# Kernel optimization log

Hardware: AMD Instinct MI355X
Metric: run time of the kernel (lower is better)

Reference implementation:

```python
import jax, jax.numpy as jnp
import numpy as np

B, S, D, H, HD, P = 2, 2048, 1024, 16, 64, 512  # batch, seq, d_model, heads, head_dim, max_pos


def setup_inputs() -> dict:
    key = jax.random.key(0)
    ks = jax.random.split(key, 7)
    s = 1.0 / np.sqrt(D)
    return {
        "hidden_states": jax.random.normal(ks[0], (B, S, D), jnp.float32),
        "Wq": jax.random.normal(ks[1], (D, D), jnp.float32) * s,
        "Wk": jax.random.normal(ks[2], (D, D), jnp.float32) * s,
        "Wv": jax.random.normal(ks[3], (D, D), jnp.float32) * s,
        "Wo": jax.random.normal(ks[4], (D, D), jnp.float32) * s,
        "bo": jnp.full((D,), 0.1, jnp.float32),
        "pos_emb": jax.random.normal(ks[5], (2 * P + 1, H), jnp.float32) * 0.02,
    }


def reference(hidden_states, Wq, Wk, Wv, Wo, bo, pos_emb):
    x = hidden_states
    b, s, d = x.shape
    # QKV projections (no bias), split heads -> [b, s, H, HD]
    q = jnp.einsum("bsd,de->bse", x, Wq).reshape(b, s, H, HD)
    k = jnp.einsum("bsd,de->bse", x, Wk).reshape(b, s, H, HD)
    v = jnp.einsum("bsd,de->bse", x, Wv).reshape(b, s, H, HD)
    # scores [b, H, i, j]
    scores = jnp.einsum("bihd,bjhd->bhij", q, k) / np.sqrt(HD) + 1e-9
    # learned relative-position bias: rel[i,j] = clamp(j - i, -P, P) + P
    pos = jnp.arange(s)
    rel = jnp.clip(pos[None, :] - pos[:, None], -P, P) + P  # [s, s] int
    bias = pos_emb[rel]  # [s, s, H]
    scores = scores + jnp.transpose(bias, (2, 0, 1))[None]  # [1,H,s,s] broadcast
    # causal mask (strict upper triangle -> -inf)
    causal = jnp.triu(jnp.ones((s, s), bool), 1)
    scores = jnp.where(causal[None, None], -jnp.inf, scores)
    probs = jax.nn.softmax(scores, axis=-1)
    # attn dropout = 0 (eval). Weighted sum over values, merge heads.
    out = jnp.einsum("bhij,bjhd->bihd", probs, v).reshape(b, s, d)
    return jnp.einsum("bsd,de->bse", out, Wo) + bo
```

## Files before the change

kernel.cpp:

```cpp
#include <hip/hip_runtime.h>
#include <math.h>

#define SEQ    2048
#define DMODEL 1024
#define NHEAD  16
#define HDIM   64
#define MAXP   512
#define NBATCH 2
#define MTOT   (NBATCH * SEQ)
#define PAD    72
#define NT     (SEQ / 64)

typedef short s16x8 __attribute__((ext_vector_type(8)));
typedef float f32x4 __attribute__((ext_vector_type(4)));

__device__ __forceinline__ unsigned short f2bf(float f) {
    unsigned u = __float_as_uint(f);
    return (unsigned short)((u + 0x7FFFu + ((u >> 16) & 1u)) >> 16);
}
__device__ __forceinline__ float bf2f(unsigned short h) {
    return __uint_as_float(((unsigned)h) << 16);
}
__device__ __forceinline__ void tsplit(float v, unsigned short& hi, unsigned short& lo) {
    unsigned u = __float_as_uint(v);
    hi = (unsigned short)(u >> 16);
    float rem = v - __uint_as_float(u & 0xFFFF0000u);
    lo = (unsigned short)(__float_as_uint(rem) >> 16);
}

__global__ __launch_bounds__(256) void split_rows(
    const float* __restrict__ in, unsigned short* __restrict__ hi,
    unsigned short* __restrict__ lo, int n4)
{
    int i = blockIdx.x * 256 + threadIdx.x;
    if (i >= n4) return;
    float4 v = ((const float4*)in)[i];
    ushort4 h, l;
    h.x = f2bf(v.x); l.x = f2bf(v.x - bf2f(h.x));
    h.y = f2bf(v.y); l.y = f2bf(v.y - bf2f(h.y));
    h.z = f2bf(v.z); l.z = f2bf(v.z - bf2f(h.z));
    h.w = f2bf(v.w); l.w = f2bf(v.w - bf2f(h.w));
    ((ushort4*)hi)[i] = h;
    ((ushort4*)lo)[i] = l;
}

__global__ __launch_bounds__(256) void split_transpose(
    const float* __restrict__ W, unsigned short* __restrict__ th,
    unsigned short* __restrict__ tl)
{
    __shared__ float tile[32][33];
    const int bx = blockIdx.x * 32;
    const int by = blockIdx.y * 32;
    const int tx = threadIdx.x & 31, ty0 = threadIdx.x >> 5;
    #pragma unroll
    for (int i = 0; i < 4; ++i) {
        int ty = ty0 + i * 8;
        tile[ty][tx] = W[(size_t)(by + ty) * DMODEL + bx + tx];
    }
    __syncthreads();
    #pragma unroll
    for (int i = 0; i < 4; ++i) {
        int ty = ty0 + i * 8;
        float v = tile[tx][ty];
        unsigned short h = f2bf(v);
        unsigned short l = f2bf(v - bf2f(h));
        size_t o = (size_t)(bx + ty) * DMODEL + by + tx;
        th[o] = h;
        tl[o] = l;
    }
}

__global__ __launch_bounds__(256, 2) void gemm_mfma(
    const unsigned short* __restrict__ Ah_g, const unsigned short* __restrict__ Al_g,
    const unsigned short* __restrict__ Bh_g, const unsigned short* __restrict__ Bl_g,
    const float* __restrict__ bias, float* __restrict__ Yf,
    unsigned short* __restrict__ Yh, unsigned short* __restrict__ Yl, int mode)
{
    __shared__ __align__(16) unsigned short Ah[128 * 32], Al[128 * 32];
    __shared__ __align__(16) unsigned short Bh[128 * 32], Bl[128 * 32];

    const int tid = threadIdx.x;
    const int lane = tid & 63, wid = tid >> 6;
    const int wr = wid >> 1, wc = wid & 1;
    const int m0 = blockIdx.y * 128, n0 = blockIdx.x * 128;

    const int srow = tid >> 2;
    const int skb = (tid & 3) * 8;
    const size_t aoff0 = (size_t)(m0 + srow) * DMODEL + skb;
    const size_t aoff1 = (size_t)(m0 + srow + 64) * DMODEL + skb;
    const size_t boff0 = (size_t)(n0 + srow) * DMODEL + skb;
    const size_t boff1 = (size_t)(n0 + srow + 64) * DMODEL + skb;
    const int lw = srow * 32 + skb;

    uint4 rah0 = *(const uint4*)(Ah_g + aoff0), rah1 = *(const uint4*)(Ah_g + aoff1);
    uint4 ral0 = *(const uint4*)(Al_g + aoff0), ral1 = *(const uint4*)(Al_g + aoff1);
    uint4 rbh0 = *(const uint4*)(Bh_g + boff0), rbh1 = *(const uint4*)(Bh_g + boff1);
    uint4 rbl0 = *(const uint4*)(Bl_g + boff0), rbl1 = *(const uint4*)(Bl_g + boff1);

    f32x4 acc[4][4] = {};

    const int fr = lane & 15;
    const int fk = (lane >> 4) * 8;

    for (int t = 0; t < DMODEL / 32; ++t) {
        __syncthreads();
        *(uint4*)&Ah[lw] = rah0; *(uint4*)&Ah[lw + 64 * 32] = rah1;
        *(uint4*)&Al[lw] = ral0; *(uint4*)&Al[lw + 64 * 32] = ral1;
        *(uint4*)&Bh[lw] = rbh0; *(uint4*)&Bh[lw + 64 * 32] = rbh1;
        *(uint4*)&Bl[lw] = rbl0; *(uint4*)&Bl[lw + 64 * 32] = rbl1;
        __syncthreads();
        if (t + 1 < DMODEL / 32) {
            const size_t ko = (size_t)(t + 1) * 32;
            rah0 = *(const uint4*)(Ah_g + aoff0 + ko);
            rah1 = *(const uint4*)(Ah_g + aoff1 + ko);
            ral0 = *(const uint4*)(Al_g + aoff0 + ko);
            ral1 = *(const uint4*)(Al_g + aoff1 + ko);
            rbh0 = *(const uint4*)(Bh_g + boff0 + ko);
            rbh1 = *(const uint4*)(Bh_g + boff1 + ko);
            rbl0 = *(const uint4*)(Bl_g + boff0 + ko);
            rbl1 = *(const uint4*)(Bl_g + boff1 + ko);
        }

        s16x8 fah[4], fal[4], fbh[4], fbl[4];
        #pragma unroll
        for (int mf = 0; mf < 4; ++mf) {
            int r = (wr * 64 + mf * 16 + fr) * 32 + fk;
            fah[mf] = *(const s16x8*)&Ah[r];
            fal[mf] = *(const s16x8*)&Al[r];
        }
        #pragma unroll
        for (int nf = 0; nf < 4; ++nf) {
            int r = (wc * 64 + nf * 16 + fr) * 32 + fk;
            fbh[nf] = *(const s16x8*)&Bh[r];
            fbl[nf] = *(const s16x8*)&Bl[r];
        }
        __builtin_amdgcn_s_setprio(1);
        #pragma unroll
        for (int mf = 0; mf < 4; ++mf)
            #pragma unroll
            for (int nf = 0; nf < 4; ++nf) {
                acc[mf][nf] = __builtin_amdgcn_mfma_f32_16x16x32_bf16(fah[mf], fbh[nf], acc[mf][nf], 0, 0, 0);
                acc[mf][nf] = __builtin_amdgcn_mfma_f32_16x16x32_bf16(fah[mf], fbl[nf], acc[mf][nf], 0, 0, 0);
                acc[mf][nf] = __builtin_amdgcn_mfma_f32_16x16x32_bf16(fal[mf], fbh[nf], acc[mf][nf], 0, 0, 0);
            }
        __builtin_amdgcn_s_setprio(0);
    }

    #pragma unroll
    for (int mf = 0; mf < 4; ++mf) {
        #pragma unroll
        for (int nf = 0; nf < 4; ++nf) {
            const int col = n0 + wc * 64 + nf * 16 + fr;
            if (mode == 2) {
                const int hh = col >> 6, d = col & 63;
                const int row0 = m0 + wr * 64 + mf * 16 + (lane >> 4) * 4;
                const int bb = row0 >> 11, ss = row0 & (SEQ - 1);
                const size_t idx = (((size_t)bb * NHEAD + hh) * HDIM + d) * SEQ + ss;
                ushort4 hv, lv;
                {
                    float v0 = acc[mf][nf][0], v1 = acc[mf][nf][1];
                    float v2 = acc[mf][nf][2], v3 = acc[mf][nf][3];
                    hv.x = f2bf(v0); lv.x = f2bf(v0 - bf2f(hv.x));
                    hv.y = f2bf(v1); lv.y = f2bf(v1 - bf2f(hv.y));
                    hv.z = f2bf(v2); lv.z = f2bf(v2 - bf2f(hv.z));
                    hv.w = f2bf(v3); lv.w = f2bf(v3 - bf2f(hv.w));
                }
                *(ushort4*)(Yh + idx) = hv;
                *(ushort4*)(Yl + idx) = lv;
            } else {
                #pragma unroll
                for (int r = 0; r < 4; ++r) {
                    const int row = m0 + wr * 64 + mf * 16 + (lane >> 4) * 4 + r;
                    const float v = acc[mf][nf][r];
                    if (mode == 0) {
                        const int hh = col >> 6, d = col & 63;
                        const int bb = row >> 11, ss = row & (SEQ - 1);
                        size_t idx = ((((size_t)bb * NHEAD + hh) * SEQ + ss) << 6) + d;
                        unsigned short hb = f2bf(v);
                        Yh[idx] = hb;
                        Yl[idx] = f2bf(v - bf2f(hb));
                    } else {
                        Yf[(size_t)row * DMODEL + col] = v + bias[col];
                    }
                }
            }
        }
    }
}

__global__ __launch_bounds__(256, 2) void attn_mfma(
    const unsigned short* __restrict__ Qh_g, const unsigned short* __restrict__ Ql_g,
    const unsigned short* __restrict__ Kh_g, const unsigned short* __restrict__ Kl_g,
    const unsigned short* __restrict__ Vth_g, const unsigned short* __restrict__ Vtl_g,
    const float* __restrict__ pos_emb,
    unsigned short* __restrict__ Oh_g, unsigned short* __restrict__ Ol_g)
{
    __shared__ __align__(16) unsigned short kph[64 * PAD];
    __shared__ __align__(16) unsigned short kpl[64 * PAD];
    __shared__ __align__(16) unsigned short vth[64 * PAD];
    __shared__ __align__(16) unsigned short vtl[64 * PAD];
    __shared__ float pe[2 * MAXP + 1];

    const int tid = threadIdx.x;
    const int lane = tid & 63, w = tid >> 6;
    const int pi = blockIdx.x, bh = blockIdx.y;
    const int b = bh >> 4, h = bh & 15;

    const size_t hboff = ((size_t)b * NHEAD + h) * SEQ * HDIM;
    const unsigned short* Qh = Qh_g + hboff;
    const unsigned short* Ql = Ql_g + hboff;
    const unsigned short* Kh = Kh_g + hboff;
    const unsigned short* Kl = Kl_g + hboff;
    const unsigned short* Vth = Vth_g + hboff;
    const unsigned short* Vtl = Vtl_g + hboff;

    for (int e = tid; e <= 2 * MAXP; e += 256)
        pe[e] = pos_emb[(size_t)e * NHEAD + h];

    const int fr = lane & 15;
    const int g = lane >> 4;
    const int fko = g * 8;

    const int strow = tid >> 3;
    const int std0 = (tid & 7) * 8;

    uint4 rkh0, rkh1, rkl0, rkl1, rvh0, rvh1, rvl0, rvl1;
#define LDREGS(J0) do {                                                         \
    const unsigned short* kp_ = Kh + (size_t)((J0) + strow) * HDIM + std0;      \
    rkh0 = *(const uint4*)kp_;  rkh1 = *(const uint4*)(kp_ + 32 * HDIM);        \
    const unsigned short* klp_ = Kl + (size_t)((J0) + strow) * HDIM + std0;     \
    rkl0 = *(const uint4*)klp_; rkl1 = *(const uint4*)(klp_ + 32 * HDIM);       \
    const unsigned short* vhp_ = Vth + (size_t)strow * SEQ + (J0) + std0;       \
    rvh0 = *(const uint4*)vhp_; rvh1 = *(const uint4*)(vhp_ + 32 * SEQ);        \
    const unsigned short* vlp_ = Vtl + (size_t)strow * SEQ + (J0) + std0;       \
    rvl0 = *(const uint4*)vlp_; rvl1 = *(const uint4*)(vlp_ + 32 * SEQ);        \
} while (0)

    for (int half = 0; half < 2; ++half) {
        const int qt = half ? (NT - 1 - pi) : pi;
        const int i0 = qt * 64;

        s16x8 qfh[2], qfl[2];
        {
            const size_t qrow = (size_t)(i0 + w * 16 + fr) * HDIM;
            qfh[0] = *(const s16x8*)(Qh + qrow + fko);
            qfh[1] = *(const s16x8*)(Qh + qrow + 32 + fko);
            qfl[0] = *(const s16x8*)(Ql + qrow + fko);
            qfl[1] = *(const s16x8*)(Ql + qrow + 32 + fko);
        }

        f32x4 oacc[4] = {};
        float mrow[4] = {-INFINITY, -INFINITY, -INFINITY, -INFINITY};
        float lrow[4] = {};

        LDREGS(0);

        for (int tj = 0; tj <= qt; ++tj) {
            const int j0 = tj * 64;
            __syncthreads();
            *(uint4*)&kph[strow * PAD + std0] = rkh0;
            *(uint4*)&kph[(strow + 32) * PAD + std0] = rkh1;
            *(uint4*)&kpl[strow * PAD + std0] = rkl0;
            *(uint4*)&kpl[(strow + 32) * PAD + std0] = rkl1;
            *(uint4*)&vth[strow * PAD + std0] = rvh0;
            *(uint4*)&vth[(strow + 32) * PAD + std0] = rvh1;
            *(uint4*)&vtl[strow * PAD + std0] = rvl0;
            *(uint4*)&vtl[(strow + 32) * PAD + std0] = rvl1;
            __syncthreads();
            if (tj < qt) LDREGS(j0 + 64);

            f32x4 s[4] = {};
            __builtin_amdgcn_s_setprio(1);
            #pragma unroll
            for (int ks = 0; ks < 2; ++ks) {
                #pragma unroll
                for (int nf = 0; nf < 4; ++nf) {
                    const int ka = (nf * 16 + fr) * PAD + ks * 32 + fko;
                    s16x8 kbh = *(const s16x8*)&kph[ka];
                    s16x8 kbl = *(const s16x8*)&kpl[ka];
                    s[nf] = __builtin_amdgcn_mfma_f32_16x16x32_bf16(qfh[ks], kbh, s[nf], 0, 0, 0);
                    s[nf] = __builtin_amdgcn_mfma_f32_16x16x32_bf16(qfh[ks], kbl, s[nf], 0, 0, 0);
                    s[nf] = __builtin_amdgcn_mfma_f32_16x16x32_bf16(qfl[ks], kbh, s[nf], 0, 0, 0);
                }
            }
            __builtin_amdgcn_s_setprio(0);
            __syncthreads();

            float mloc[4] = {-INFINITY, -INFINITY, -INFINITY, -INFINITY};
            if (qt - tj >= 9) {
                const float c0 = 1e-9f + pe[0];
                #pragma unroll
                for (int nf = 0; nf < 4; ++nf)
                    #pragma unroll
                    for (int r = 0; r < 4; ++r) {
                        float sv = s[nf][r] * 0.125f + c0;
                        s[nf][r] = sv;
                        mloc[r] = fmaxf(mloc[r], sv);
                    }
            } else if (tj < qt) {
                #pragma unroll
                for (int nf = 0; nf < 4; ++nf) {
                    const int jg = j0 + nf * 16 + fr;
                    #pragma unroll
                    for (int r = 0; r < 4; ++r) {
                        const int ig = i0 + w * 16 + g * 4 + r;
                        int rel = jg - ig;
                        rel = rel < -MAXP ? -MAXP : rel;
                        float sv = s[nf][r] * 0.125f + 1e-9f + pe[rel + MAXP];
                        s[nf][r] = sv;
                        mloc[r] = fmaxf(mloc[r], sv);
                    }
                }
            } else {
                #pragma unroll
                for (int nf = 0; nf < 4; ++nf) {
                    const int jg = j0 + nf * 16 + fr;
                    #pragma unroll
                    for (int r = 0; r < 4; ++r) {
                        const int ig = i0 + w * 16 + g * 4 + r;
                        float sv = s[nf][r] * 0.125f + 1e-9f + pe[jg - ig + MAXP];
                        sv = (jg > ig) ? -INFINITY : sv;
                        s[nf][r] = sv;
                        mloc[r] = fmaxf(mloc[r], sv);
                    }
                }
            }

            float lsum[4];
            #pragma unroll
            for (int r = 0; r < 4; ++r) {
                float mx = mloc[r];
                #pragma unroll
                for (int msk = 1; msk < 16; msk <<= 1)
                    mx = fmaxf(mx, __shfl_xor(mx, msk, 64));
                const float mnew = fmaxf(mrow[r], mx);
                const float fac = __expf(mrow[r] - mnew);
                mrow[r] = mnew;
                lrow[r] *= fac;
                #pragma unroll
                for (int nf = 0; nf < 4; ++nf) oacc[nf][r] *= fac;
                lsum[r] = 0.f;
            }
            #pragma unroll
            for (int nf = 0; nf < 4; ++nf) {
                #pragma unroll
                for (int r = 0; r < 4; ++r) {
                    const float p = __expf(s[nf][r] - mrow[r]);
                    lsum[r] += p;
                    unsigned short hb, lb;
                    tsplit(p, hb, lb);
                    const int idx = (w * 16 + g * 4 + r) * PAD + nf * 16 + fr;
                    kph[idx] = hb;
                    kpl[idx] = lb;
                }
            }
            #pragma unroll
            for (int r = 0; r < 4; ++r) {
                float ls = lsum[r];
                #pragma unroll
                for (int msk = 1; msk < 16; msk <<= 1)
                    ls += __shfl_xor(ls, msk, 64);
                lrow[r] += ls;
            }

            __builtin_amdgcn_s_setprio(1);
            #pragma unroll
            for (int ks = 0; ks < 2; ++ks) {
                const int pa = (w * 16 + fr) * PAD + ks * 32 + fko;
                s16x8 pah = *(const s16x8*)&kph[pa];
                s16x8 pal = *(const s16x8*)&kpl[pa];
                #pragma unroll
                for (int nf = 0; nf < 4; ++nf) {
                    const int va = (nf * 16 + fr) * PAD + ks * 32 + fko;
                    s16x8 vbh = *(const s16x8*)&vth[va];
                    s16x8 vbl = *(const s16x8*)&vtl[va];
                    oacc[nf] = __builtin_amdgcn_mfma_f32_16x16x32_bf16(pah, vbh, oacc[nf], 0, 0, 0);
                    oacc[nf] = __builtin_amdgcn_mfma_f32_16x16x32_bf16(pah, vbl, oacc[nf], 0, 0, 0);
                    oacc[nf] = __builtin_amdgcn_mfma_f32_16x16x32_bf16(pal, vbh, oacc[nf], 0, 0, 0);
                }
            }
            __builtin_amdgcn_s_setprio(0);
        }

        float inv[4];
        #pragma unroll
        for (int r = 0; r < 4; ++r) inv[r] = 1.0f / lrow[r];
        #pragma unroll
        for (int nf = 0; nf < 4; ++nf) {
            #pragma unroll
            for (int r = 0; r < 4; ++r) {
                const size_t m = (size_t)b * SEQ + i0 + w * 16 + g * 4 + r;
                const size_t idx = m * DMODEL + h * HDIM + nf * 16 + fr;
                unsigned short hv, lv;
                tsplit(oacc[nf][r] * inv[r], hv, lv);
                Oh_g[idx] = hv;
                Ol_g[idx] = lv;
            }
        }
    }
#undef LDREGS
}

extern "C" void kernel_launch(void* const* d_in, const int* in_sizes, int n_in,
                              void* d_out, int out_size, void* d_ws, size_t ws_size,
                              hipStream_t stream) {
    const float* x   = (const float*)d_in[0];
    const float* Wq  = (const float*)d_in[1];
    const float* Wk  = (const float*)d_in[2];
    const float* Wv  = (const float*)d_in[3];
    const float* Wo  = (const float*)d_in[4];
    const float* bo  = (const float*)d_in[5];
    const float* pem = (const float*)d_in[6];
    float* out = (float*)d_out;

    char* w = (char*)d_ws;
    const size_t MB = 1 << 20;
    unsigned short* oh  = (unsigned short*)(w + 0 * MB);
    unsigned short* ol  = (unsigned short*)(w + 8 * MB);
    unsigned short* qh  = (unsigned short*)(w + 16 * MB);
    unsigned short* ql  = (unsigned short*)(w + 24 * MB);
    unsigned short* kh  = (unsigned short*)(w + 32 * MB);
    unsigned short* kl  = (unsigned short*)(w + 40 * MB);
    unsigned short* vth = (unsigned short*)(w + 48 * MB);
    unsigned short* vtl = (unsigned short*)(w + 56 * MB);
    unsigned short* Xh  = (unsigned short*)(w + 64 * MB);
    unsigned short* Xl  = (unsigned short*)(w + 72 * MB);
    unsigned short* Wqh = (unsigned short*)(w + 80 * MB);
    unsigned short* Wql = (unsigned short*)(w + 82 * MB);
    unsigned short* Wkh = (unsigned short*)(w + 84 * MB);
    unsigned short* Wkl = (unsigned short*)(w + 86 * MB);
    unsigned short* Wvh = (unsigned short*)(w + 88 * MB);
    unsigned short* Wvl = (unsigned short*)(w + 90 * MB);
    unsigned short* Woh = (unsigned short*)(w + 92 * MB);
    unsigned short* Wol = (unsigned short*)(w + 94 * MB);

    const int nX4 = MTOT * DMODEL / 4;
    split_rows<<<dim3(nX4 / 256), 256, 0, stream>>>(x, Xh, Xl, nX4);

    dim3 tg(32, 32);
    split_transpose<<<tg, 256, 0, stream>>>(Wq, Wqh, Wql);
    split_transpose<<<tg, 256, 0, stream>>>(Wk, Wkh, Wkl);
    split_transpose<<<tg, 256, 0, stream>>>(Wv, Wvh, Wvl);
    split_transpose<<<tg, 256, 0, stream>>>(Wo, Woh, Wol);

    dim3 gg(DMODEL / 128, MTOT / 128);
    gemm_mfma<<<gg, 256, 0, stream>>>(Xh, Xl, Wqh, Wql, nullptr, nullptr, qh, ql, 0);
    gemm_mfma<<<gg, 256, 0, stream>>>(Xh, Xl, Wkh, Wkl, nullptr, nullptr, kh, kl, 0);
    gemm_mfma<<<gg, 256, 0, stream>>>(Xh, Xl, Wvh, Wvl, nullptr, nullptr, vth, vtl, 2);

    attn_mfma<<<dim3(NT / 2, NBATCH * NHEAD), 256, 0, stream>>>(
        qh, ql, kh, kl, vth, vtl, pem, oh, ol);

    gemm_mfma<<<gg, 256, 0, stream>>>(oh, ol, Woh, Wol, bo, out, nullptr, nullptr, 1);
}
```

Before: 389.2 us.

## Fuse QKV GEMMs, use direct global-to-LDS loads, restructure attention softmax layout

Merges the three QKV projection launches into one grid that selects the weight by block column, and replaces register-staged prefetching with global_load_lds direct copies into shared memory. Occupancy hint raised to 3. The attention kernel swaps MFMA operand order so each lane holds one query row, which cuts the shuffle reductions for the online softmax. P gets its own LDS buffers, removing a barrier, and LDS padding shrinks to 68. The GEMM no longer overlaps the next tile's load with compute, and the new padding may misalign 16-byte LDS reads.

```diff
diff --git a/kernel.cpp b/kernel.cpp
--- a/kernel.cpp
+++ b/kernel.cpp
@@ -8,11 +8,18 @@
 #define MAXP   512
 #define NBATCH 2
 #define MTOT   (NBATCH * SEQ)
-#define PAD    72
+#define PAD    68
 #define NT     (SEQ / 64)
 
 typedef short s16x8 __attribute__((ext_vector_type(8)));
 typedef float f32x4 __attribute__((ext_vector_type(4)));
+
+typedef unsigned int u32_as1 __attribute__((address_space(1)));
+typedef unsigned int u32_as3 __attribute__((address_space(3)));
+
+__device__ __forceinline__ void gload16(const void* g, void* l) {
+    __builtin_amdgcn_global_load_lds((const u32_as1*)g, (u32_as3*)l, 16, 0, 0);
+}
 
 __device__ __forceinline__ unsigned short f2bf(float f) {
     unsigned u = __float_as_uint(f);
@@ -70,11 +77,16 @@
     }
 }
 
-__global__ __launch_bounds__(256, 2) void gemm_mfma(
+__global__ __launch_bounds__(256, 3) void gemm_mfma(
     const unsigned short* __restrict__ Ah_g, const unsigned short* __restrict__ Al_g,
-    const unsigned short* __restrict__ Bh_g, const unsigned short* __restrict__ Bl_g,
+    const unsigned short* __restrict__ B0h, const unsigned short* __restrict__ B0l,
+    const unsigned short* __restrict__ B1h, const unsigned short* __restrict__ B1l,
+    const unsigned short* __restrict__ B2h, const unsigned short* __restrict__ B2l,
     const float* __restrict__ bias, float* __restrict__ Yf,
-    unsigned short* __restrict__ Yh, unsigned short* __restrict__ Yl, int mode)
+    unsigned short* __restrict__ Y0h, unsigned short* __restrict__ Y0l,
+    unsigned short* __restrict__ Y1h, unsigned short* __restrict__ Y1l,
+    unsigned short* __restrict__ Y2h, unsigned short* __restrict__ Y2l,
+    int mode)
 {
     __shared__ __align__(16) unsigned short Ah[128 * 32], Al[128 * 32];
     __shared__ __align__(16) unsigned short Bh[128 * 32], Bl[128 * 32];
@@ -82,44 +94,33 @@
     const int tid = threadIdx.x;
     const int lane = tid & 63, wid = tid >> 6;
     const int wr = wid >> 1, wc = wid & 1;
-    const int m0 = blockIdx.y * 128, n0 = blockIdx.x * 128;
-
-    const int srow = tid >> 2;
-    const int skb = (tid & 3) * 8;
-    const size_t aoff0 = (size_t)(m0 + srow) * DMODEL + skb;
-    const size_t aoff1 = (size_t)(m0 + srow + 64) * DMODEL + skb;
-    const size_t boff0 = (size_t)(n0 + srow) * DMODEL + skb;
-    const size_t boff1 = (size_t)(n0 + srow + 64) * DMODEL + skb;
-    const int lw = srow * 32 + skb;
-
-    uint4 rah0 = *(const uint4*)(Ah_g + aoff0), rah1 = *(const uint4*)(Ah_g + aoff1);
-    uint4 ral0 = *(const uint4*)(Al_g + aoff0), ral1 = *(const uint4*)(Al_g + aoff1);
-    uint4 rbh0 = *(const uint4*)(Bh_g + boff0), rbh1 = *(const uint4*)(Bh_g + boff1);
-    uint4 rbl0 = *(const uint4*)(Bl_g + boff0), rbl1 = *(const uint4*)(Bl_g + boff1);
+    const int m0 = blockIdx.y * 128;
+    const int which = (mode == 0) ? (blockIdx.x >> 3) : 0;
+    const int n0 = ((mode == 0) ? (blockIdx.x & 7) : blockIdx.x) * 128;
+
+    const unsigned short* Bh_g = (which == 0) ? B0h : (which == 1 ? B1h : B2h);
+    const unsigned short* Bl_g = (which == 0) ? B0l : (which == 1 ? B1l : B2l);
+
+    const size_t aoff0 = (size_t)(m0 + wid * 16 + (lane >> 2)) * DMODEL + (lane & 3) * 8;
+    const size_t boff0 = (size_t)(n0 + wid * 16 + (lane >> 2)) * DMODEL + (lane & 3) * 8;
+    const int ldsw = wid * 512;
 
     f32x4 acc[4][4] = {};
-
     const int fr = lane & 15;
     const int fk = (lane >> 4) * 8;
 
     for (int t = 0; t < DMODEL / 32; ++t) {
+        const size_t ko = (size_t)t * 32;
         __syncthreads();
-        *(uint4*)&Ah[lw] = rah0; *(uint4*)&Ah[lw + 64 * 32] = rah1;
-        *(uint4*)&Al[lw] = ral0; *(uint4*)&Al[lw + 64 * 32] = ral1;
-        *(uint4*)&Bh[lw] = rbh0; *(uint4*)&Bh[lw + 64 * 32] = rbh1;
-        *(uint4*)&Bl[lw] = rbl0; *(uint4*)&Bl[lw + 64 * 32] = rbl1;
+        gload16(Ah_g + aoff0 + ko, &Ah[ldsw]);
+        gload16(Ah_g + aoff0 + (size_t)64 * DMODEL + ko, &Ah[2048 + ldsw]);
+        gload16(Al_g + aoff0 + ko, &Al[ldsw]);
+        gload16(Al_g + aoff0 + (size_t)64 * DMODEL + ko, &Al[2048 + ldsw]);
+        gload16(Bh_g + boff0 + ko, &Bh[ldsw]);
+        gload16(Bh_g + boff0 + (size_t)64 * DMODEL + ko, &Bh[2048 + ldsw]);
+        gload16(Bl_g + boff0 + ko, &Bl[ldsw]);
+        gload16(Bl_g + boff0 + (size_t)64 * DMODEL + ko, &Bl[2048 + ldsw]);
         __syncthreads();
-        if (t + 1 < DMODEL / 32) {
-            const size_t ko = (size_t)(t + 1) * 32;
-            rah0 = *(const uint4*)(Ah_g + aoff0 + ko);
-            rah1 = *(const uint4*)(Ah_g + aoff1 + ko);
-            ral0 = *(const uint4*)(Al_g + aoff0 + ko);
-            ral1 = *(const uint4*)(Al_g + aoff1 + ko);
-            rbh0 = *(const uint4*)(Bh_g + boff0 + ko);
-            rbh1 = *(const uint4*)(Bh_g + boff1 + ko);
-            rbl0 = *(const uint4*)(Bl_g + boff0 + ko);
-            rbl1 = *(const uint4*)(Bl_g + boff1 + ko);
-        }
 
         s16x8 fah[4], fal[4], fbh[4], fbl[4];
         #pragma unroll
@@ -151,37 +152,37 @@
         #pragma unroll
         for (int nf = 0; nf < 4; ++nf) {
             const int col = n0 + wc * 64 + nf * 16 + fr;
-            if (mode == 2) {
+            if (mode == 1) {
+                #pragma unroll
+                for (int r = 0; r < 4; ++r) {
+                    const int row = m0 + wr * 64 + mf * 16 + (lane >> 4) * 4 + r;
+                    Yf[(size_t)row * DMODEL + col] = acc[mf][nf][r] + bias[col];
+                }
+            } else if (which == 2) {
                 const int hh = col >> 6, d = col & 63;
                 const int row0 = m0 + wr * 64 + mf * 16 + (lane >> 4) * 4;
                 const int bb = row0 >> 11, ss = row0 & (SEQ - 1);
                 const size_t idx = (((size_t)bb * NHEAD + hh) * HDIM + d) * SEQ + ss;
                 ushort4 hv, lv;
-                {
-                    float v0 = acc[mf][nf][0], v1 = acc[mf][nf][1];
-                    float v2 = acc[mf][nf][2], v3 = acc[mf][nf][3];
-                    hv.x = f2bf(v0); lv.x = f2bf(v0 - bf2f(hv.x));
-                    hv.y = f2bf(v1); lv.y = f2bf(v1 - bf2f(hv.y));
-                    hv.z = f2bf(v2); lv.z = f2bf(v2 - bf2f(hv.z));
-                    hv.w = f2bf(v3); lv.w = f2bf(v3 - bf2f(hv.w));
-                }
-                *(ushort4*)(Yh + idx) = hv;
-                *(ushort4*)(Yl + idx) = lv;
+                tsplit(acc[mf][nf][0], hv.x, lv.x);
+                tsplit(acc[mf][nf][1], hv.y, lv.y);
+                tsplit(acc[mf][nf][2], hv.z, lv.z);
+                tsplit(acc[mf][nf][3], hv.w, lv.w);
+                *(ushort4*)(Y2h + idx) = hv;
+                *(ushort4*)(Y2l + idx) = lv;
             } else {
+                unsigned short* Yh = which ? Y1h : Y0h;
+                unsigned short* Yl = which ? Y1l : Y0l;
+                const int hh = col >> 6, d = col & 63;
                 #pragma unroll
                 for (int r = 0; r < 4; ++r) {
                     const int row = m0 + wr * 64 + mf * 16 + (lane >> 4) * 4 + r;
-                    const float v = acc[mf][nf][r];
-                    if (mode == 0) {
-                        const int hh = col >> 6, d = col & 63;
-                        const int bb = row >> 11, ss = row & (SEQ - 1);
-                        size_t idx = ((((size_t)bb * NHEAD + hh) * SEQ + ss) << 6) + d;
-                        unsigned short hb = f2bf(v);
-                        Yh[idx] = hb;
-                        Yl[idx] = f2bf(v - bf2f(hb));
-                    } else {
-                        Yf[(size_t)row * DMODEL + col] = v + bias[col];
-                    }
+                    const int bb = row >> 11, ss = row & (SEQ - 1);
+                    const size_t idx = ((((size_t)bb * NHEAD + hh) * SEQ + ss) << 6) + d;
+                    unsigned short hb, lb;
+                    tsplit(acc[mf][nf][r], hb, lb);
+                    Yh[idx] = hb;
+                    Yl[idx] = lb;
                 }
             }
         }
@@ -195,10 +196,9 @@
     const float* __restrict__ pos_emb,
     unsigned short* __restrict__ Oh_g, unsigned short* __restrict__ Ol_g)
 {
-    __shared__ __align__(16) unsigned short kph[64 * PAD];
-    __shared__ __align__(16) unsigned short kpl[64 * PAD];
-    __shared__ __align__(16) unsigned short vth[64 * PAD];
-    __shared__ __align__(16) unsigned short vtl[64 * PAD];
+    __shared__ __align__(16) unsigned short klh[64 * PAD], kll[64 * PAD];
+    __shared__ __align__(16) unsigned short vth[64 * PAD], vtl[64 * PAD];
+    __shared__ __align__(16) unsigned short plh[64 * PAD], pll[64 * PAD];
     __shared__ float pe[2 * MAXP + 1];
 
     const int tid = threadIdx.x;
@@ -216,6 +216,8 @@
 
     for (int e = tid; e <= 2 * MAXP; e += 256)
         pe[e] = pos_emb[(size_t)e * NHEAD + h];
+    __syncthreads();
+    const float pe0 = pe[0];
 
     const int fr = lane & 15;
     const int g = lane >> 4;
@@ -239,6 +241,7 @@
     for (int half = 0; half < 2; ++half) {
         const int qt = half ? (NT - 1 - pi) : pi;
         const int i0 = qt * 64;
+        const int ig = i0 + w * 16 + fr;
 
         s16x8 qfh[2], qfl[2];
         {
@@ -250,18 +253,17 @@
         }
 
         f32x4 oacc[4] = {};
-        float mrow[4] = {-INFINITY, -INFINITY, -INFINITY, -INFINITY};
-        float lrow[4] = {};
+        float m_r = -INFINITY, l_r = 0.f;
 
         LDREGS(0);
 
         for (int tj = 0; tj <= qt; ++tj) {
             const int j0 = tj * 64;
             __syncthreads();
-            *(uint4*)&kph[strow * PAD + std0] = rkh0;
-            *(uint4*)&kph[(strow + 32) * PAD + std0] = rkh1;
-            *(uint4*)&kpl[strow * PAD + std0] = rkl0;
-            *(uint4*)&kpl[(strow + 32) * PAD + std0] = rkl1;
+            *(uint4*)&klh[strow * PAD + std0] = rkh0;
+            *(uint4*)&klh[(strow + 32) * PAD + std0] = rkh1;
+            *(uint4*)&kll[strow * PAD + std0] = rkl0;
+            *(uint4*)&kll[(strow + 32) * PAD + std0] = rkl1;
             *(uint4*)&vth[strow * PAD + std0] = rvh0;
             *(uint4*)&vth[(strow + 32) * PAD + std0] = rvh1;
             *(uint4*)&vtl[strow * PAD + std0] = rvl0;
@@ -276,99 +278,94 @@
                 #pragma unroll
                 for (int nf = 0; nf < 4; ++nf) {
                     const int ka = (nf * 16 + fr) * PAD + ks * 32 + fko;
-                    s16x8 kbh = *(const s16x8*)&kph[ka];
-                    s16x8 kbl = *(const s16x8*)&kpl[ka];
-                    s[nf] = __builtin_amdgcn_mfma_f32_16x16x32_bf16(qfh[ks], kbh, s[nf], 0, 0, 0);
-                    s[nf] = __builtin_amdgcn_mfma_f32_16x16x32_bf16(qfh[ks], kbl, s[nf], 0, 0, 0);
-                    s[nf] = __builtin_amdgcn_mfma_f32_16x16x32_bf16(qfl[ks], kbh, s[nf], 0, 0, 0);
+                    s16x8 kbh = *(const s16x8*)&klh[ka];
+                    s16x8 kbl = *(const s16x8*)&kll[ka];
+                    s[nf] = __builtin_amdgcn_mfma_f32_16x16x32_bf16(kbh, qfh[ks], s[nf], 0, 0, 0);
+                    s[nf] = __builtin_amdgcn_mfma_f32_16x16x32_bf16(kbl, qfh[ks], s[nf], 0, 0, 0);
+                    s[nf] = __builtin_amdgcn_mfma_f32_16x16x32_bf16(kbh, qfl[ks], s[nf], 0, 0, 0);
                 }
             }
             __builtin_amdgcn_s_setprio(0);
-            __syncthreads();
-
-            float mloc[4] = {-INFINITY, -INFINITY, -INFINITY, -INFINITY};
+
+            float pmax = -INFINITY;
             if (qt - tj >= 9) {
-                const float c0 = 1e-9f + pe[0];
+                const float c0 = 1e-9f + pe0;
                 #pragma unroll
                 for (int nf = 0; nf < 4; ++nf)
                     #pragma unroll
                     for (int r = 0; r < 4; ++r) {
-                        float sv = s[nf][r] * 0.125f + c0;
+                        const float sv = s[nf][r] * 0.125f + c0;
                         s[nf][r] = sv;
-                        mloc[r] = fmaxf(mloc[r], sv);
+                        pmax = fmaxf(pmax, sv);
                     }
             } else if (tj < qt) {
                 #pragma unroll
                 for (int nf = 0; nf < 4; ++nf) {
-                    const int jg = j0 + nf * 16 + fr;
+                    const int jb = j0 + nf * 16 + g * 4;
                     #pragma unroll
                     for (int r = 0; r < 4; ++r) {
-                        const int ig = i0 + w * 16 + g * 4 + r;
-                        int rel = jg - ig;
+                        int rel = jb + r - ig;
                         rel = rel < -MAXP ? -MAXP : rel;
-                        float sv = s[nf][r] * 0.125f + 1e-9f + pe[rel + MAXP];
+                        const float sv = s[nf][r] * 0.125f + 1e-9f + pe[rel + MAXP];
                         s[nf][r] = sv;
-                        mloc[r] = fmaxf(mloc[r], sv);
+                        pmax = fmaxf(pmax, sv);
                     }
                 }
             } else {
                 #pragma unroll
                 for (int nf = 0; nf < 4; ++nf) {
-                    const int jg = j0 + nf * 16 + fr;
+                    const int jb = j0 + nf * 16 + g * 4;
                     #pragma unroll
                     for (int r = 0; r < 4; ++r) {
-                        const int ig = i0 + w * 16 + g * 4 + r;
+                        const int jg = jb + r;
                         float sv = s[nf][r] * 0.125f + 1e-9f + pe[jg - ig + MAXP];
                         sv = (jg > ig) ? -INFINITY : sv;
                         s[nf][r] = sv;
-                        mloc[r] = fmaxf(mloc[r], sv);
+                        pmax = fmaxf(pmax, sv);
                     }
                 }
             }
-
-            float lsum[4];
+            pmax = fmaxf(pmax, __shfl_xor(pmax, 16, 64));
+            pmax = fmaxf(pmax, __shfl_xor(pmax, 32, 64));
+            const float mnew = fmaxf(m_r, pmax);
+            const float fac = __expf(m_r - mnew);
+            m_r = mnew;
+            float lsum = 0.f;
+            #pragma unroll
+            for (int nf = 0; nf < 4; ++nf)
+                #pragma unroll
+                for (int r = 0; r < 4; ++r) {
+                    const float p = __expf(s[nf][r] - mnew);
+                    s[nf][r] = p;
+                    lsum += p;
+                }
+            lsum += __shfl_xor(lsum, 16, 64);
+            lsum += __shfl_xor(lsum, 32, 64);
+            l_r = l_r * fac + lsum;
             #pragma unroll
             for (int r = 0; r < 4; ++r) {
-                float mx = mloc[r];
-                #pragma unroll
-                for (int msk = 1; msk < 16; msk <<= 1)
-                    mx = fmaxf(mx, __shfl_xor(mx, msk, 64));
-                const float mnew = fmaxf(mrow[r], mx);
-                const float fac = __expf(mrow[r] - mnew);
-                mrow[r] = mnew;
-                lrow[r] *= fac;
-                #pragma unroll
-                for (int nf = 0; nf < 4; ++nf) oacc[nf][r] *= fac;
-                lsum[r] = 0.f;
-            }
+                const float facq = __shfl(fac, g * 4 + r, 64);
+                #pragma unroll
+                for (int nf = 0; nf < 4; ++nf) oacc[nf][r] *= facq;
+            }
+            const int prow = (w * 16 + fr) * PAD;
             #pragma unroll
             for (int nf = 0; nf < 4; ++nf) {
-                #pragma unroll
-                for (int r = 0; r < 4; ++r) {
-                    const float p = __expf(s[nf][r] - mrow[r]);
-                    lsum[r] += p;
-                    unsigned short hb, lb;
-                    tsplit(p, hb, lb);
-                    const int idx = (w * 16 + g * 4 + r) * PAD + nf * 16 + fr;
-                    kph[idx] = hb;
-                    kpl[idx] = lb;
-                }
-            }
-            #pragma unroll
-            for (int r = 0; r < 4; ++r) {
-                float ls = lsum[r];
-                #pragma unroll
-                for (int msk = 1; msk < 16; msk <<= 1)
-                    ls += __shfl_xor(ls, msk, 64);
-                lrow[r] += ls;
+                ushort4 h4, l4;
+                tsplit(s[nf][0], h4.x, l4.x);
+                tsplit(s[nf][1], h4.y, l4.y);
+                tsplit(s[nf][2], h4.z, l4.z);
+                tsplit(s[nf][3], h4.w, l4.w);
+                *(ushort4*)&plh[prow + nf * 16 + g * 4] = h4;
+                *(ushort4*)&pll[prow + nf * 16 + g * 4] = l4;
             }
 
             __builtin_amdgcn_s_setprio(1);
             #pragma unroll
             for (int ks = 0; ks < 2; ++ks) {
-                const int pa = (w * 16 + fr) * PAD + ks * 32 + fko;
-                s16x8 pah = *(const s16x8*)&kph[pa];
-                s16x8 pal = *(const s16x8*)&kpl[pa];
+                const int pa = prow + ks * 32 + fko;
+                s16x8 pah = *(const s16x8*)&plh[pa];
+                s16x8 pal = *(const s16x8*)&pll[pa];
                 #pragma unroll
                 for (int nf = 0; nf < 4; ++nf) {
                     const int va = (nf * 16 + fr) * PAD + ks * 32 + fko;
@@ -382,17 +379,16 @@
             __builtin_amdgcn_s_setprio(0);
         }
 
-        float inv[4];
+        const float linv = 1.0f / l_r;
         #pragma unroll
-        for (int r = 0; r < 4; ++r) inv[r] = 1.0f / lrow[r];
-        #pragma unroll
-        for (int nf = 0; nf < 4; ++nf) {
-            #pragma unroll
-            for (int r = 0; r < 4; ++r) {
-                const size_t m = (size_t)b * SEQ + i0 + w * 16 + g * 4 + r;
+        for (int r = 0; r < 4; ++r) {
+            const float invq = __shfl(linv, g * 4 + r, 64);
+            const size_t m = (size_t)b * SEQ + i0 + w * 16 + g * 4 + r;
+            #pragma unroll
+            for (int nf = 0; nf < 4; ++nf) {
                 const size_t idx = m * DMODEL + h * HDIM + nf * 16 + fr;
                 unsigned short hv, lv;
-                tsplit(oacc[nf][r] * inv[r], hv, lv);
+                tsplit(oacc[nf][r] * invq, hv, lv);
                 Oh_g[idx] = hv;
                 Ol_g[idx] = lv;
             }
@@ -443,13 +439,18 @@
     split_transpose<<<tg, 256, 0, stream>>>(Wv, Wvh, Wvl);
     split_transpose<<<tg, 256, 0, stream>>>(Wo, Woh, Wol);
 
-    dim3 gg(DMODEL / 128, MTOT / 128);
-    gemm_mfma<<<gg, 256, 0, stream>>>(Xh, Xl, Wqh, Wql, nullptr, nullptr, qh, ql, 0);
-    gemm_mfma<<<gg, 256, 0, stream>>>(Xh, Xl, Wkh, Wkl, nullptr, nullptr, kh, kl, 0);
-    gemm_mfma<<<gg, 256, 0, stream>>>(Xh, Xl, Wvh, Wvl, nullptr, nullptr, vth, vtl, 2);
+    dim3 gq(24, MTOT / 128);
+    gemm_mfma<<<gq, 256, 0, stream>>>(Xh, Xl,
+                                      Wqh, Wql, Wkh, Wkl, Wvh, Wvl,
+                                      nullptr, nullptr,
+                                      qh, ql, kh, kl, vth, vtl, 0);
 
     attn_mfma<<<dim3(NT / 2, NBATCH * NHEAD), 256, 0, stream>>>(
         qh, ql, kh, kl, vth, vtl, pem, oh, ol);
 
-    gemm_mfma<<<gg, 256, 0, stream>>>(oh, ol, Woh, Wol, bo, out, nullptr, nullptr, 1);
-}
+    dim3 go(DMODEL / 128, MTOT / 128);
+    gemm_mfma<<<go, 256, 0, stream>>>(oh, ol,
+                                      Woh, Wol, nullptr, nullptr, nullptr, nullptr,
+                                      bo, out,
+                                      nullptr, nullptr, nullptr, nullptr, nullptr, nullptr, 1);
+}
```

Result: faster. 316.1 us (-18.8%).
